# Kernel optimization log

Measured on AMD Instinct MI355X. Metric: run time of the kernel, lower is better.

## Reference

```python
import jax, jax.numpy as jnp
import numpy as np

SQRT_D = 16.0   # sqrt(d), d=256
BETA2 = 18.0    # beta^2 / 2, beta=6
EPS_BN = 1e-5


def _bn1d(x, g, b):
    # eval-mode BatchNorm1d with freshly-initialized running stats (mean=0, var=1)
    scale = g / jnp.sqrt(1.0 + EPS_BN)
    if x.ndim == 3:  # [B, C, N]
        return x * scale[:, None] + b[:, None]
    return x * scale + b  # [B, C]


def _crelu(z):
    return jax.nn.relu(z.real) + 1j * jax.nn.relu(z.imag)


def _sa_layer(x, qk_w, v_w, v_b, t_w, t_b, g, b):
    # x: [B, C, N]; q and k share weights (q_conv.weight = k_conv.weight)
    xq = jnp.einsum('oc,bcn->bno', qk_w, x)            # [B, N, C/4]
    xk = jnp.einsum('oc,bcn->bon', qk_w, x)            # [B, C/4, N]
    xv = jnp.einsum('oc,bcn->bon', v_w, x) + v_b[:, None]
    energy = jnp.einsum('bno,bom->bnm', xq, xk)        # [B, N, N]
    att = jax.nn.softmax(energy, axis=-1)
    att = att / (1e-9 + att.sum(axis=1, keepdims=True))  # sum-normalized over dim=1
    xr = jnp.einsum('bcn,bnm->bcm', xv, att)           # [B, C, N]
    xr = jax.nn.relu(_bn1d(jnp.einsum('oc,bcn->bon', t_w, x - xr) + t_b[:, None], g, b))
    return x + xr


def _forward(x, A, P, cl1_wr, cl1_wi, cl1_br, cl1_bi, cl2_wr, cl2_wi, cl2_br, cl2_bi,
             pt_conv1_w, pt_conv2_w, pt_bn1_g, pt_bn1_b, pt_bn2_g, pt_bn2_b,
             sa_qk_w, sa_v_w, sa_v_b, sa_t_w, sa_t_b, sa_bn_g, sa_bn_b,
             fuse_w, fuse_bn_g, fuse_bn_b, lin1_w, bn6_g, bn6_b,
             lin2_w, lin2_b, bn7_g, bn7_b, lin3_w, lin3_b):
    pts = jnp.transpose(x, (0, 2, 1))                  # [B, N, 3]
    # ---- VecKM: pairwise Gaussian kernel times complex random features ----
    sq = jnp.sum(pts * pts, axis=-1)                   # [B, N]
    D2 = sq[:, :, None] + sq[:, None, :] - 2.0 * jnp.einsum('bnc,bmc->bnm', pts, pts)
    J = jnp.exp(-BETA2 * D2).astype(jnp.complex64)     # [B, N, N]
    eA = jnp.exp(1j * (pts @ A))                       # [B, N, d] complex64
    G = (J @ eA) / eA
    G = G / jnp.linalg.norm(G, axis=-1, keepdims=True) * SQRT_D
    G = G + jnp.exp(1j * (pts @ P))                    # positional encoding
    # ---- ComplexLinear -> ComplexReLU -> ComplexLinear ----
    W1 = (cl1_wr + 1j * cl1_wi).astype(jnp.complex64)
    G = _crelu(G @ W1.T + (cl1_br + 1j * cl1_bi))
    W2 = (cl2_wr + 1j * cl2_wi).astype(jnp.complex64)
    G = G @ W2.T + (cl2_br + 1j * cl2_bi)
    Gr = G.real ** 2 + G.imag ** 2                     # [B, N, 256]
    Gc = jnp.transpose(Gr, (0, 2, 1))                  # [B, 256, N]
    # ---- Point_Transformer_Last ----
    h = jax.nn.relu(_bn1d(jnp.einsum('oc,bcn->bon', pt_conv1_w, Gc), pt_bn1_g, pt_bn1_b))
    h = jax.nn.relu(_bn1d(jnp.einsum('oc,bcn->bon', pt_conv2_w, h), pt_bn2_g, pt_bn2_b))
    feats = []
    for i in range(4):
        h = _sa_layer(h, sa_qk_w[i], sa_v_w[i], sa_v_b[i], sa_t_w[i], sa_t_b[i],
                      sa_bn_g[i], sa_bn_b[i])
        feats.append(h)
    h = jnp.concatenate(feats + [Gc], axis=1)          # [B, 1280, N]
    h = jax.nn.leaky_relu(_bn1d(jnp.einsum('oc,bcn->bon', fuse_w, h), fuse_bn_g, fuse_bn_b), 0.2)
    h = jnp.max(h, axis=-1)                            # adaptive_max_pool1d -> [B, 1024]
    h = jax.nn.leaky_relu(_bn1d(h @ lin1_w.T, bn6_g, bn6_b), 0.2)
    h = jax.nn.leaky_relu(_bn1d(h @ lin2_w.T + lin2_b, bn7_g, bn7_b), 0.2)
    return h @ lin3_w.T + lin3_b                       # [B, 40]


def setup_inputs() -> dict:
    key = jax.random.key(0)
    ks = iter(jax.random.split(key, 64))
    B, N, d = 16, 1024, 256
    r = lambda shape, s=0.05: jax.random.normal(next(ks), shape, dtype=jnp.float32) * s
    inp = {
        'x': jax.random.normal(next(ks), (B, 3, N), dtype=jnp.float32),
        'A': jax.random.normal(next(ks), (3, d), dtype=jnp.float32) * 30.0,
        'P': jax.random.normal(next(ks), (3, d), dtype=jnp.float32),
        'cl1_wr': r((d, d)), 'cl1_wi': r((d, d)), 'cl1_br': r((d,)), 'cl1_bi': r((d,)),
        'cl2_wr': r((d, d)), 'cl2_wi': r((d, d)), 'cl2_br': r((d,)), 'cl2_bi': r((d,)),
        'pt_conv1_w': r((256, 256)), 'pt_conv2_w': r((256, 256)),
        'pt_bn1_g': jnp.ones(256), 'pt_bn1_b': jnp.zeros(256),
        'pt_bn2_g': jnp.ones(256), 'pt_bn2_b': jnp.zeros(256),
        'sa_qk_w': r((4, 64, 256)), 'sa_v_w': r((4, 256, 256)), 'sa_v_b': r((4, 256)),
        'sa_t_w': r((4, 256, 256)), 'sa_t_b': r((4, 256)),
        'sa_bn_g': jnp.ones((4, 256)), 'sa_bn_b': jnp.zeros((4, 256)),
        'fuse_w': r((1024, 1280)), 'fuse_bn_g': jnp.ones(1024), 'fuse_bn_b': jnp.zeros(1024),
        'lin1_w': r((512, 1024)), 'bn6_g': jnp.ones(512), 'bn6_b': jnp.zeros(512),
        'lin2_w': r((256, 512)), 'lin2_b': r((256,)),
        'bn7_g': jnp.ones(256), 'bn7_b': jnp.zeros(256),
        'lin3_w': r((40, 256)), 'lin3_b': r((40,)),
    }
    return inp


def reference(x, A, P, cl1_wr, cl1_wi, cl1_br, cl1_bi, cl2_wr, cl2_wi, cl2_br, cl2_bi,
              pt_conv1_w, pt_conv2_w, pt_bn1_g, pt_bn1_b, pt_bn2_g, pt_bn2_b,
              sa_qk_w, sa_v_w, sa_v_b, sa_t_w, sa_t_b, sa_bn_g, sa_bn_b,
              fuse_w, fuse_bn_g, fuse_bn_b, lin1_w, bn6_g, bn6_b,
              lin2_w, lin2_b, bn7_g, bn7_b, lin3_w, lin3_b):
    return _forward(x, A, P, cl1_wr, cl1_wi, cl1_br, cl1_bi, cl2_wr, cl2_wi, cl2_br, cl2_bi,
                    pt_conv1_w, pt_conv2_w, pt_bn1_g, pt_bn1_b, pt_bn2_g, pt_bn2_b,
                    sa_qk_w, sa_v_w, sa_v_b, sa_t_w, sa_t_b, sa_bn_g, sa_bn_b,
                    fuse_w, fuse_bn_g, fuse_bn_b, lin1_w, bn6_g, bn6_b,
                    lin2_w, lin2_b, bn7_g, bn7_b, lin3_w, lin3_b)
```

## Files before the change

kernel.cpp:

```cpp
#include <hip/hip_runtime.h>
#include <math.h>

#define BB 16
#define NN 1024
#define DD 256

typedef unsigned short u16;
typedef unsigned int uint32;
typedef __attribute__((ext_vector_type(8))) short s8v;
typedef __attribute__((ext_vector_type(4))) float f4v;

__device__ __forceinline__ u16 f2b(float f) {
  uint32 u = __float_as_uint(f);
  return (u16)((u + 0x7fffu + ((u >> 16) & 1u)) >> 16);
}
__device__ __forceinline__ float b2f(u16 u) {
  return __uint_as_float(((uint32)u) << 16);
}

__device__ __forceinline__ float waveRedSum(float v) {
  #pragma unroll
  for (int o = 32; o; o >>= 1) v += __shfl_xor(v, o, 64);
  return v;
}
__device__ __forceinline__ float waveRedMax(float v) {
  #pragma unroll
  for (int o = 32; o; o >>= 1) v = fmaxf(v, __shfl_xor(v, o, 64));
  return v;
}

__global__ void k_pts(const float* __restrict__ x, float* __restrict__ pts) {
  int i = blockIdx.x * 256 + threadIdx.x;
  if (i >= BB * NN) return;
  int b = i >> 10, n = i & 1023;
  const float* xb = x + (size_t)b * 3 * NN;
  pts[i * 3 + 0] = xb[n];
  pts[i * 3 + 1] = xb[NN + n];
  pts[i * 3 + 2] = xb[2 * NN + n];
}

__global__ void k_phase(const float* __restrict__ pts, const float* __restrict__ A,
                        float2* __restrict__ eA) {
  int i = blockIdx.x * 256 + threadIdx.x;
  int d = i & 255; int bn = i >> 8;
  float p0 = pts[bn * 3], p1 = pts[bn * 3 + 1], p2 = pts[bn * 3 + 2];
  float ta = p0 * A[d] + p1 * A[256 + d] + p2 * A[512 + d];
  float s, c;
  sincosf(ta, &s, &c); eA[i] = make_float2(c, s);
}

__global__ void k_eat(const float2* __restrict__ eA, u16* __restrict__ eAT) {
  int bid = blockIdx.x;
  int dt = bid & 7, nt = (bid >> 3) & 15, b = bid >> 7;
  int d0 = dt * 32, n0 = nt * 64;
  __shared__ u16 cosT[32][72], sinT[32][72];
  int t = threadIdx.x;
  {
    int n = t >> 2, dg = (t & 3) * 8;
    const float2* p = eA + ((size_t)(b * 1024 + n0 + n)) * 256 + d0 + dg;
    #pragma unroll
    for (int j = 0; j < 8; j++) {
      float2 v = p[j];
      cosT[dg + j][n] = f2b(v.x);
      sinT[dg + j][n] = f2b(v.y);
    }
  }
  __syncthreads();
  {
    int rr = t >> 2, ng = (t & 3) * 16;
    int d = rr >> 1, cmp = rr & 1;
    const u16* src = (cmp ? &sinT[d][ng] : &cosT[d][ng]);
    uint4 v0 = *(const uint4*)src;
    uint4 v1 = *(const uint4*)(src + 8);
    u16* dst = eAT + ((size_t)(b * 512 + 2 * d0 + rr)) * 1024 + n0 + ng;
    *(uint4*)dst = v0;
    *(uint4*)(dst + 8) = v1;
  }
}

__global__ void k_jbuild(const float* __restrict__ pts, u16* __restrict__ J) {
  int bid = blockIdx.x;
  int b = bid >> 10, n = bid & 1023;
  int t = threadIdx.x;
  const float* pb = pts + (size_t)b * 3072;
  float pnx = pb[n * 3], pny = pb[n * 3 + 1], pnz = pb[n * 3 + 2];
  int m = t * 4;
  const float* pm = pb + (size_t)m * 3;
  float4 a = *(const float4*)pm;
  float4 bq = *(const float4*)(pm + 4);
  float4 c = *(const float4*)(pm + 8);
  float dx, dy, dz, d2;
  dx = a.x - pnx;  dy = a.y - pny;  dz = a.z - pnz;  d2 = dx*dx + dy*dy + dz*dz;
  float j0 = __expf(-18.0f * d2);
  dx = a.w - pnx;  dy = bq.x - pny; dz = bq.y - pnz; d2 = dx*dx + dy*dy + dz*dz;
  float j1 = __expf(-18.0f * d2);
  dx = bq.z - pnx; dy = bq.w - pny; dz = c.x - pnz;  d2 = dx*dx + dy*dy + dz*dz;
  float j2 = __expf(-18.0f * d2);
  dx = c.y - pnx;  dy = c.z - pny;  dz = c.w - pnz;  d2 = dx*dx + dy*dy + dz*dz;
  float j3 = __expf(-18.0f * d2);
  uint32 lo = (uint32)f2b(j0) | ((uint32)f2b(j1) << 16);
  uint32 hi = (uint32)f2b(j2) | ((uint32)f2b(j3) << 16);
  *(uint2*)(J + (size_t)bid * 1024 + m) = make_uint2(lo, hi);
}

__global__ void k_norm(const float2* __restrict__ M, const float2* __restrict__ eA,
                       const float* __restrict__ pts, const float* __restrict__ P,
                       u16* __restrict__ Gb) {
  int bn = blockIdx.x; int c = threadIdx.x;
  size_t idx = (size_t)bn * DD + c;
  float2 m = M[idx], e = eA[idx];
  float gr = m.x * e.x + m.y * e.y;
  float gi = m.y * e.x - m.x * e.y;
  float s = gr * gr + gi * gi;
  s = waveRedSum(s);
  __shared__ float red[4];
  if ((c & 63) == 0) red[c >> 6] = s;
  __syncthreads();
  float tot = red[0] + red[1] + red[2] + red[3];
  float scale = 16.0f / sqrtf(tot);
  float p0 = pts[bn * 3], p1 = pts[bn * 3 + 1], p2 = pts[bn * 3 + 2];
  float tp = p0 * P[c] + p1 * P[256 + c] + p2 * P[512 + c];
  float sp, cp; sincosf(tp, &sp, &cp);
  uint32 pk = (uint32)f2b(gr * scale + cp) | ((uint32)f2b(gi * scale + sp) << 16);
  *(uint32*)(Gb + idx * 2) = pk;
}

__global__ void k_cast(const float* __restrict__ s, u16* __restrict__ d, int n) {
  int i = blockIdx.x * 256 + threadIdx.x;
  if (i < n) d[i] = f2b(s[i]);
}
__global__ void k_wprep(const float* __restrict__ wr, const float* __restrict__ wi,
                        u16* __restrict__ dst) {
  int i = blockIdx.x * 256 + threadIdx.x;
  int op = i >> 9, c2 = i & 511, c = c2 >> 1, pl = c2 & 1;
  float v;
  if (op < 256) v = pl ? -wi[op * 256 + c] : wr[op * 256 + c];
  else          v = pl ?  wr[(op - 256) * 256 + c] : wi[(op - 256) * 256 + c];
  dst[i] = f2b(v);
}
__global__ void k_cbias(const float* __restrict__ br, const float* __restrict__ bi,
                        float* __restrict__ cb) {
  int t = threadIdx.x;
  cb[t] = (t < 256) ? br[t] : bi[t - 256];
}

__global__ void k_g2(const u16* __restrict__ G2b, u16* __restrict__ bigT) {
  int i = blockIdx.x * 256 + threadIdx.x;
  int row = i >> 8, c = i & 255;
  float re = b2f(G2b[(size_t)row * 512 + 2 * c]);
  float im = b2f(G2b[(size_t)row * 512 + 2 * c + 1]);
  bigT[(size_t)row * 1280 + 1024 + c] = f2b(re * re + im * im);
}

template<int BM>
__launch_bounds__(256)
__global__ void k_mm(const u16* __restrict__ Ab, long a_bs, int lda,
                     const u16* __restrict__ Btb, long b_bs, int ldb,
                     int K, int tiles_m, int tiles_n,
                     const float* __restrict__ bias,
                     const float* __restrict__ bng, const float* __restrict__ bnb,
                     const float* __restrict__ cbias,
                     int act,
                     const float* __restrict__ res, long res_bs, int res_sub,
                     float* __restrict__ outF, long outF_bs, int ldF,
                     u16* __restrict__ outB, long outB_bs, int ldBo, int ileave,
                     u16* __restrict__ outT, long outT_bs, int ldT) {
  constexpr int BN = 128;
  constexpr int WM = (BM == 128) ? 64 : 32;
  constexpr int MI = WM / 16;
  __shared__ u16 smem[BN * BM];
  u16* As = smem;
  u16* Bs = smem + BM * 32;
  int t = threadIdx.x;
  int l = t & 63, w = t >> 6;
  int p = l & 15, q = l >> 4;
  int bid = blockIdx.x;
  int tn = bid % tiles_n;
  int tm = (bid / tiles_n) % tiles_m;
  int b  = bid / (tiles_n * tiles_m);
  int m0 = tm * BM, n0 = tn * BN;
  int wm = w >> 1, wn = w & 1;
  const u16* Ap = Ab + (size_t)b * a_bs;
  const u16* Bp = Btb + (size_t)b * b_bs;

  f4v acc[MI][4];
  #pragma unroll
  for (int i = 0; i < MI; i++)
    #pragma unroll
    for (int j = 0; j < 4; j++) acc[i][j] = (f4v){0.f, 0.f, 0.f, 0.f};

  int arow = t >> 2, kg = (t & 3) * 8;
  for (int k0 = 0; k0 < K; k0 += 32) {
    __syncthreads();
    #pragma unroll
    for (int it = 0; it < BM / 64; it++) {
      int r = it * 64 + arow;
      float4 v = *(const float4*)(Ap + (size_t)(m0 + r) * lda + k0 + kg);
      *(float4*)&As[r * 32 + kg] = v;
    }
    #pragma unroll
    for (int it = 0; it < 2; it++) {
      int r = it * 64 + arow;
      float4 v = *(const float4*)(Bp + (size_t)(n0 + r) * ldb + k0 + kg);
      *(float4*)&Bs[r * 32 + kg] = v;
    }
    __syncthreads();
    s8v af[MI], bf[4];
    #pragma unroll
    for (int i = 0; i < MI; i++)
      af[i] = *(const s8v*)&As[(wm * WM + i * 16 + p) * 32 + q * 8];
    #pragma unroll
    for (int j = 0; j < 4; j++)
      bf[j] = *(const s8v*)&Bs[(wn * 64 + j * 16 + p) * 32 + q * 8];
    #pragma unroll
    for (int i = 0; i < MI; i++)
      #pragma unroll
      for (int j = 0; j < 4; j++)
        acc[i][j] = __builtin_amdgcn_mfma_f32_16x16x32_bf16(af[i], bf[j], acc[i][j], 0, 0, 0);
  }

  __syncthreads();

  float cbv[4];
  #pragma unroll
  for (int j = 0; j < 4; j++) {
    int no = n0 + wn * 64 + j * 16 + p;
    cbv[j] = cbias ? cbias[no] : 0.0f;
  }
  const float BNS = 0.99999500003749966f;
  #pragma unroll
  for (int i = 0; i < MI; i++) {
    #pragma unroll
    for (int r = 0; r < 4; r++) {
      int mo = m0 + wm * WM + i * 16 + q * 4 + r;
      float mult = 1.f, add = 0.f;
      if (bias) add = bias[mo];
      if (bng) { float s = bng[mo] * BNS; add = add * s + bnb[mo]; mult = s; }
      #pragma unroll
      for (int j = 0; j < 4; j++) {
        int no = n0 + wn * 64 + j * 16 + p;
        float v = acc[i][j][r];
        v = v * mult + add;
        if (cbias) v += cbv[j];
        if (act == 1) v = fmaxf(v, 0.f);
        else if (act == 2) v = v > 0.f ? v : 0.2f * v;
        if (res) {
          float rv = res[(size_t)b * res_bs + (size_t)mo * NN + no];
          v = res_sub ? rv - v : rv + v;
        }
        if (outF) outF[(size_t)b * outF_bs + (size_t)mo * ldF + no] = v;
        if (outB) {
          int noo = ileave ? (((no & 255) << 1) | (no >> 8)) : no;
          outB[(size_t)b * outB_bs + (size_t)mo * ldBo + noo] = f2b(v);
        }
        if (outT) smem[(wn * 64 + j * 16 + p) * BM + (mo - m0)] = f2b(v);
      }
    }
  }
  if (outT) {
    __syncthreads();
    constexpr int CPR = BM / 8;
    constexpr int RPP = 256 / CPR;
    int row0 = t / CPR, cg = (t % CPR) * 8;
    for (int rr = row0; rr < BN; rr += RPP) {
      float4 v = *(const float4*)&smem[rr * BM + cg];
      *(float4*)(outT + (size_t)b * outT_bs + (size_t)(n0 + rr) * ldT + m0 + cg) = v;
    }
  }
}

__global__ void k_rowstats(const float* __restrict__ E, float* __restrict__ rmax_,
                           float* __restrict__ rinv_) {
  int row = blockIdx.x;
  const float* pp = E + (size_t)row * NN;
  int t = threadIdx.x;
  float4 v = *(const float4*)(pp + t * 4);
  float mx = fmaxf(fmaxf(v.x, v.y), fmaxf(v.z, v.w));
  mx = waveRedMax(mx);
  __shared__ float redm[4];
  __shared__ float reds[4];
  if ((t & 63) == 0) redm[t >> 6] = mx;
  __syncthreads();
  mx = fmaxf(fmaxf(redm[0], redm[1]), fmaxf(redm[2], redm[3]));
  float s = __expf(v.x - mx) + __expf(v.y - mx) + __expf(v.z - mx) + __expf(v.w - mx);
  s = waveRedSum(s);
  if ((t & 63) == 0) reds[t >> 6] = s;
  __syncthreads();
  if (t == 0) {
    float tot = reds[0] + reds[1] + reds[2] + reds[3];
    rmax_[row] = mx;
    rinv_[row] = 1.0f / tot;
  }
}

__launch_bounds__(256)
__global__ void k_xratt(const u16* __restrict__ xv_, const float* __restrict__ E,
                        const float* __restrict__ rmax_, const float* __restrict__ rinv_,
                        const float* __restrict__ XinF, long xinF_bs,
                        u16* __restrict__ diffT) {
  __shared__ u16 smem[16384];
  __shared__ float colred[128][4];
  u16* As = smem;
  u16* Bs = smem + 4096;
  int t = threadIdx.x;
  int l = t & 63, w = t >> 6;
  int p = l & 15, q = l >> 4;
  int bid = blockIdx.x;
  int mt = bid & 7, ct = (bid >> 3) & 1, b = bid >> 4;
  int c0 = ct * 128, m0 = mt * 128;
  int wm = w >> 1, wn = w & 1;
  const u16* Ap = xv_ + (size_t)b * 262144;
  const float* Ep = E + ((size_t)b << 20);
  const float* rmx = rmax_ + (b << 10);
  const float* riv = rinv_ + (b << 10);
  f4v acc[4][4];
  #pragma unroll
  for (int i = 0; i < 4; i++)
    #pragma unroll
    for (int j = 0; j < 4; j++) acc[i][j] = (f4v){0.f, 0.f, 0.f, 0.f};
  float colpart0 = 0.f, colpart1 = 0.f;
  int arow = t >> 2, kg = (t & 3) * 8;
  for (int k0 = 0; k0 < 1024; k0 += 32) {
    __syncthreads();
    #pragma unroll
    for (int it = 0; it < 2; it++) {
      int r = it * 64 + arow;
      *(float4*)&As[r * 32 + kg] = *(const float4*)(Ap + (size_t)(c0 + r) * 1024 + k0 + kg);
    }
    float4 ma0 = *(const float4*)(rmx + k0 + kg);
    float4 ma1 = *(const float4*)(rmx + k0 + kg + 4);
    float4 ia0 = *(const float4*)(riv + k0 + kg);
    float4 ia1 = *(const float4*)(riv + k0 + kg + 4);
    #pragma unroll
    for (int it = 0; it < 2; it++) {
      int r = it * 64 + arow;
      const float* ep = Ep + (size_t)(m0 + r) * 1024 + k0 + kg;
      float4 e0 = *(const float4*)ep;
      float4 e1 = *(const float4*)(ep + 4);
      float p0 = __expf(e0.x - ma0.x) * ia0.x;
      float p1 = __expf(e0.y - ma0.y) * ia0.y;
      float p2 = __expf(e0.z - ma0.z) * ia0.z;
      float p3 = __expf(e0.w - ma0.w) * ia0.w;
      float p4 = __expf(e1.x - ma1.x) * ia1.x;
      float p5 = __expf(e1.y - ma1.y) * ia1.y;
      float p6 = __expf(e1.z - ma1.z) * ia1.z;
      float p7 = __expf(e1.w - ma1.w) * ia1.w;
      float s8 = ((p0 + p1) + (p2 + p3)) + ((p4 + p5) + (p6 + p7));
      if (it == 0) colpart0 += s8; else colpart1 += s8;
      uint32 w0 = (uint32)f2b(p0) | ((uint32)f2b(p1) << 16);
      uint32 w1 = (uint32)f2b(p2) | ((uint32)f2b(p3) << 16);
      uint32 w2 = (uint32)f2b(p4) | ((uint32)f2b(p5) << 16);
      uint32 w3 = (uint32)f2b(p6) | ((uint32)f2b(p7) << 16);
      *(uint4*)&Bs[r * 32 + kg] = make_uint4(w0, w1, w2, w3);
    }
    __syncthreads();
    s8v af[4], bf[4];
    #pragma unroll
    for (int i = 0; i < 4; i++)
      af[i] = *(const s8v*)&As[(wm * 64 + i * 16 + p) * 32 + q * 8];
    #pragma unroll
    for (int j = 0; j < 4; j++)
      bf[j] = *(const s8v*)&Bs[(wn * 64 + j * 16 + p) * 32 + q * 8];
    #pragma unroll
    for (int i = 0; i < 4; i++)
      #pragma unroll
      for (int j = 0; j < 4; j++)
        acc[i][j] = __builtin_amdgcn_mfma_f32_16x16x32_bf16(af[i], bf[j], acc[i][j], 0, 0, 0);
  }
  colred[arow][t & 3] = colpart0;
  colred[64 + arow][t & 3] = colpart1;
  __syncthreads();
  float csv[4];
  #pragma unroll
  for (int j = 0; j < 4; j++) {
    int ml = wn * 64 + j * 16 + p;
    csv[j] = 1.0f / (1e-9f + colred[ml][0] + colred[ml][1] + colred[ml][2] + colred[ml][3]);
  }
  #pragma unroll
  for (int i = 0; i < 4; i++) {
    #pragma unroll
    for (int r = 0; r < 4; r++) {
      int cl = wm * 64 + i * 16 + q * 4 + r;
      int c = c0 + cl;
      #pragma unroll
      for (int j = 0; j < 4; j++) {
        int ml = wn * 64 + j * 16 + p;
        float v = acc[i][j][r] * csv[j];
        float rv = XinF[(size_t)b * xinF_bs + (size_t)c * 1024 + m0 + ml];
        smem[ml * 128 + cl] = f2b(rv - v);
      }
    }
  }
  __syncthreads();
  int rr0 = t >> 4, cg = (t & 15) * 8;
  #pragma unroll
  for (int k = 0; k < 8; k++) {
    int rr = rr0 + k * 16;
    *(float4*)(diffT + (size_t)b * 262144 + (size_t)(m0 + rr) * 256 + c0 + cg) =
        *(const float4*)&smem[rr * 128 + cg];
  }
}

__global__ void k_maxpool(const float* __restrict__ fin, float* __restrict__ pool) {
  int bo = blockIdx.x;
  const float* pp = fin + (size_t)bo * NN;
  int t = threadIdx.x;
  float m = fmaxf(fmaxf(pp[t], pp[t + 256]), fmaxf(pp[t + 512], pp[t + 768]));
  m = waveRedMax(m);
  __shared__ float red[4];
  if ((t & 63) == 0) red[t >> 6] = m;
  __syncthreads();
  if (t == 0) pool[bo] = fmaxf(fmaxf(red[0], red[1]), fmaxf(red[2], red[3]));
}

__global__ void k_fc(const float* __restrict__ in, int Cc,
                     const float* __restrict__ W,
                     const float* __restrict__ bias,
                     const float* __restrict__ bng, const float* __restrict__ bnb,
                     int act, float* __restrict__ out, int O) {
  int i = blockIdx.x * 256 + threadIdx.x;
  if (i >= BB * O) return;
  int b = i / O, o = i % O;
  const float* xp = in + (size_t)b * Cc;
  const float* wp = W + (size_t)o * Cc;
  float s = 0.f;
  for (int c = 0; c < Cc; c += 4) {
    float4 xv = *(const float4*)(xp + c);
    float4 wv = *(const float4*)(wp + c);
    s += xv.x * wv.x + xv.y * wv.y + xv.z * wv.z + xv.w * wv.w;
  }
  if (bias) s += bias[o];
  const float BNS = 0.99999500003749966f;
  if (bng) s = s * (bng[o] * BNS) + bnb[o];
  if (act == 2) s = s > 0.f ? s : 0.2f * s;
  else if (act == 1) s = fmaxf(s, 0.f);
  out[i] = s;
}

extern "C" void kernel_launch(void* const* d_in, const int* in_sizes, int n_in,
                              void* d_out, int out_size, void* d_ws, size_t ws_size,
                              hipStream_t stream) {
  const float* x        = (const float*)d_in[0];
  const float* A        = (const float*)d_in[1];
  const float* P        = (const float*)d_in[2];
  const float* cl1_wr   = (const float*)d_in[3];
  const float* cl1_wi   = (const float*)d_in[4];
  const float* cl1_br   = (const float*)d_in[5];
  const float* cl1_bi   = (const float*)d_in[6];
  const float* cl2_wr   = (const float*)d_in[7];
  const float* cl2_wi   = (const float*)d_in[8];
  const float* cl2_br   = (const float*)d_in[9];
  const float* cl2_bi   = (const float*)d_in[10];
  const float* pt_c1_w  = (const float*)d_in[11];
  const float* pt_c2_w  = (const float*)d_in[12];
  const float* pt_bn1_g = (const float*)d_in[13];
  const float* pt_bn1_b = (const float*)d_in[14];
  const float* pt_bn2_g = (const float*)d_in[15];
  const float* pt_bn2_b = (const float*)d_in[16];
  const float* sa_qk_w  = (const float*)d_in[17];
  const float* sa_v_w   = (const float*)d_in[18];
  const float* sa_v_b   = (const float*)d_in[19];
  const float* sa_t_w   = (const float*)d_in[20];
  const float* sa_t_b   = (const float*)d_in[21];
  const float* sa_bn_g  = (const float*)d_in[22];
  const float* sa_bn_b  = (const float*)d_in[23];
  const float* fuse_w   = (const float*)d_in[24];
  const float* fuse_g   = (const float*)d_in[25];
  const float* fuse_b   = (const float*)d_in[26];
  const float* lin1_w   = (const float*)d_in[27];
  const float* bn6_g    = (const float*)d_in[28];
  const float* bn6_b    = (const float*)d_in[29];
  const float* lin2_w   = (const float*)d_in[30];
  const float* lin2_b   = (const float*)d_in[31];
  const float* bn7_g    = (const float*)d_in[32];
  const float* bn7_b    = (const float*)d_in[33];
  const float* lin3_w   = (const float*)d_in[34];
  const float* lin3_b   = (const float*)d_in[35];

  float* ws = (float*)d_ws;
  const size_t oPts  = 0;
  const size_t oS    = 65536;
  const size_t oBigT = oS + 16777216;
  const size_t oXf0  = oBigT + 10485760;
  const size_t oXf1  = oXf0 + 4194304;
  const size_t oH1T  = oXf1 + 4194304;
  const size_t oH2T  = oH1T + 2097152;
  const size_t oXkT  = oH2T + 2097152;
  const size_t oXv   = oXkT + 524288;
  const size_t oAux  = oXv + 2097152;
  const size_t oGb   = oAux + 8388608;
  const size_t oW1c  = oGb + 4194304;
  const size_t oW2c  = oW1c + 131072;
  const size_t oCb1  = oW2c + 131072;
  const size_t oCb2  = oCb1 + 512;
  const size_t oPool = oCb2 + 512;
  const size_t oFc1  = oPool + 16384;
  const size_t oFc2  = oFc1 + 8192;
  const size_t oWp   = oFc2 + 4096;

  float*  pts  = ws + oPts;
  float2* eA   = (float2*)(ws + oS);
  float2* Mj   = (float2*)(ws + oS + 8388608);
  u16*    G1b  = (u16*)(ws + oS);
  u16*    G2b  = (u16*)(ws + oS + 8388608);
  float*  Ebuf = ws + oS;
  float*  fuseO= ws + oS;
  u16*    bigT = (u16*)(ws + oBigT);
  float*  Xf0  = ws + oXf0;
  float*  Xf1  = ws + oXf1;
  u16*    h1T  = (u16*)(ws + oH1T);
  u16*    diffT= (u16*)(ws + oH1T);
  u16*    h2T  = (u16*)(ws + oH2T);
  u16*    xkT  = (u16*)(ws + oXkT);
  u16*    xv   = (u16*)(ws + oXv);
  u16*    eAT  = (u16*)(ws + oAux);
  u16*    Jb   = (u16*)(ws + oAux + 4194304);
  float*  rmax = ws + oAux;
  float*  rinv = ws + oAux + 16384;
  u16*    Gb   = (u16*)(ws + oGb);
  u16*    W1c  = (u16*)(ws + oW1c);
  u16*    W2c  = (u16*)(ws + oW2c);
  float*  cb1  = ws + oCb1;
  float*  cb2  = ws + oCb2;
  float*  pool = ws + oPool;
  float*  fc1  = ws + oFc1;
  float*  fc2  = ws + oFc2;
  u16*    wp   = (u16*)(ws + oWp);
  u16* wp_pt1  = wp;
  u16* wp_pt2  = wp + 65536;
  u16* wp_qk   = wp + 131072;
  u16* wp_v    = wp + 196608;
  u16* wp_t    = wp + 458752;
  u16* wp_fuse = wp + 720896;

  k_cast<<<256, 256, 0, stream>>>(pt_c1_w, wp_pt1, 65536);
  k_cast<<<256, 256, 0, stream>>>(pt_c2_w, wp_pt2, 65536);
  k_cast<<<256, 256, 0, stream>>>(sa_qk_w, wp_qk, 65536);
  k_cast<<<1024, 256, 0, stream>>>(sa_v_w, wp_v, 262144);
  k_cast<<<1024, 256, 0, stream>>>(sa_t_w, wp_t, 262144);
  k_cast<<<5120, 256, 0, stream>>>(fuse_w, wp_fuse, 1310720);
  k_wprep<<<1024, 256, 0, stream>>>(cl1_wr, cl1_wi, W1c);
  k_wprep<<<1024, 256, 0, stream>>>(cl2_wr, cl2_wi, W2c);
  k_cbias<<<1, 512, 0, stream>>>(cl1_br, cl1_bi, cb1);
  k_cbias<<<1, 512, 0, stream>>>(cl2_br, cl2_bi, cb2);

  k_pts<<<64, 256, 0, stream>>>(x, pts);
  k_phase<<<16384, 256, 0, stream>>>(pts, A, eA);
  k_eat<<<2048, 256, 0, stream>>>(eA, eAT);
  k_jbuild<<<16384, 256, 0, stream>>>(pts, Jb);
  k_mm<128><<<512, 256, 0, stream>>>(Jb, 1048576, 1024, eAT, 524288, 1024, 1024, 8, 4,
      nullptr, nullptr, nullptr, nullptr, 0, nullptr, 0, 0,
      (float*)Mj, 524288, 512, nullptr, 0, 0, 0, nullptr, 0, 0);
  k_norm<<<BB * NN, 256, 0, stream>>>(Mj, eA, pts, P, Gb);

  k_mm<128><<<512, 256, 0, stream>>>(Gb, 0, 512, W1c, 0, 512, 512, 128, 4,
      nullptr, nullptr, nullptr, cb1, 1, nullptr, 0, 0,
      nullptr, 0, 0, G1b, 0, 512, 1, nullptr, 0, 0);
  k_mm<128><<<512, 256, 0, stream>>>(G1b, 0, 512, W2c, 0, 512, 512, 128, 4,
      nullptr, nullptr, nullptr, cb2, 0, nullptr, 0, 0,
      nullptr, 0, 0, G2b, 0, 512, 1, nullptr, 0, 0);
  k_g2<<<16384, 256, 0, stream>>>(G2b, bigT);

  const long bsBigT = 1310720;
  const long bsH256 = 262144;
  const long bsXkT  = 65536;
  const long bsXvU  = 262144;
  const long bsF    = 262144;
  const long bsE    = 1048576;

  k_mm<128><<<256, 256, 0, stream>>>(wp_pt1, 0, 256, bigT + 1024, bsBigT, 1280, 256, 2, 8,
      nullptr, pt_bn1_g, pt_bn1_b, nullptr, 1, nullptr, 0, 0,
      nullptr, 0, 0, nullptr, 0, 0, 0, h1T, bsH256, 256);
  k_mm<128><<<256, 256, 0, stream>>>(wp_pt2, 0, 256, h1T, bsH256, 256, 256, 2, 8,
      nullptr, pt_bn2_g, pt_bn2_b, nullptr, 1, nullptr, 0, 0,
      Xf0, bsF, 1024, nullptr, 0, 0, 0, h2T, bsH256, 256);

  for (int i = 0; i < 4; i++) {
    const u16* XinT   = (i == 0) ? h2T : (bigT + (i - 1) * 256);
    long       xinT_bs= (i == 0) ? bsH256 : bsBigT;
    int        xinT_ld= (i == 0) ? 256 : 1280;
    float*     XinF   = (i & 1) ? Xf1 : Xf0;
    float*     XoutF  = (i & 1) ? Xf0 : Xf1;
    const u16* qkw = wp_qk + (size_t)i * 16384;
    const u16* vw  = wp_v + (size_t)i * 65536;
    const u16* tw  = wp_t + (size_t)i * 65536;

    k_mm<64><<<128, 256, 0, stream>>>(qkw, 0, 256, XinT, xinT_bs, xinT_ld, 256, 1, 8,
        nullptr, nullptr, nullptr, nullptr, 0, nullptr, 0, 0,
        nullptr, 0, 0, nullptr, 0, 0, 0, xkT, bsXkT, 64);
    k_mm<128><<<256, 256, 0, stream>>>(vw, 0, 256, XinT, xinT_bs, xinT_ld, 256, 2, 8,
        sa_v_b + i * 256, nullptr, nullptr, nullptr, 0, nullptr, 0, 0,
        nullptr, 0, 0, xv, bsXvU, 1024, 0, nullptr, 0, 0);
    k_mm<128><<<1024, 256, 0, stream>>>(xkT, bsXkT, 64, xkT, bsXkT, 64, 64, 8, 8,
        nullptr, nullptr, nullptr, nullptr, 0, nullptr, 0, 0,
        Ebuf, bsE, 1024, nullptr, 0, 0, 0, nullptr, 0, 0);
    k_rowstats<<<BB * NN, 256, 0, stream>>>(Ebuf, rmax, rinv);
    k_xratt<<<256, 256, 0, stream>>>(xv, Ebuf, rmax, rinv, XinF, bsF, diffT);
    k_mm<128><<<256, 256, 0, stream>>>(tw, 0, 256, diffT, bsH256, 256, 256, 2, 8,
        sa_t_b + i * 256, sa_bn_g + i * 256, sa_bn_b + i * 256, nullptr, 1,
        XinF, bsF, 0,
        XoutF, bsF, 1024, nullptr, 0, 0, 0, bigT + i * 256, bsBigT, 1280);
  }

  k_mm<128><<<1024, 256, 0, stream>>>(wp_fuse, 0, 1280, bigT, bsBigT, 1280, 1280, 8, 8,
      nullptr, fuse_g, fuse_b, nullptr, 2, nullptr, 0, 0,
      fuseO, 1048576, 1024, nullptr, 0, 0, 0, nullptr, 0, 0);
  k_maxpool<<<BB * 1024, 256, 0, stream>>>(fuseO, pool);

  k_fc<<<32, 256, 0, stream>>>(pool, 1024, lin1_w, nullptr, bn6_g, bn6_b, 2, fc1, 512);
  k_fc<<<16, 256, 0, stream>>>(fc1, 512, lin2_w, lin2_b, bn7_g, bn7_b, 2, fc2, 256);
  k_fc<<<3, 256, 0, stream>>>(fc2, 256, lin3_w, lin3_b, nullptr, nullptr, 0, (float*)d_out, 40);
}
```

Measured before the change: 1.096 ms.

## Recompute attention energy on the fly and fuse max-pool into fuse GEMM

The full N×N energy matrix is no longer written to memory. Row softmax statistics now come from a tiled MFMA kernel that emits per-tile partial max/sum, followed by a small combine kernel. The attention-times-value kernel recomputes energy tiles from xkT with MFMA instead of reading the stored fp32 energy. The fuse GEMM reduces its output tile to per-row maxima, so the 1024-wide fuse output is never stored, and a tiny kernel finishes the pool. LDS rows in the GEMM are padded to reduce bank conflicts. The cost is redundant energy MFMA work and more kernel complexity.

After: 1.535 ms. 1.4x slower.

```diff
diff --git a/kernel.cpp b/kernel.cpp
--- a/kernel.cpp
+++ b/kernel.cpp
@@ -164,13 +164,15 @@
                      const float* __restrict__ res, long res_bs, int res_sub,
                      float* __restrict__ outF, long outF_bs, int ldF,
                      u16* __restrict__ outB, long outB_bs, int ldBo, int ileave,
-                     u16* __restrict__ outT, long outT_bs, int ldT) {
+                     u16* __restrict__ outT, long outT_bs, int ldT,
+                     float* __restrict__ outPool) {
   constexpr int BN = 128;
   constexpr int WM = (BM == 128) ? 64 : 32;
   constexpr int MI = WM / 16;
-  __shared__ u16 smem[BN * BM];
+  constexpr int TLD = BM + 8;
+  __shared__ u16 smem[BN * TLD];
   u16* As = smem;
-  u16* Bs = smem + BM * 32;
+  u16* Bs = smem + BM * 36;
   int t = threadIdx.x;
   int l = t & 63, w = t >> 6;
   int p = l & 15, q = l >> 4;
@@ -196,22 +198,22 @@
     for (int it = 0; it < BM / 64; it++) {
       int r = it * 64 + arow;
       float4 v = *(const float4*)(Ap + (size_t)(m0 + r) * lda + k0 + kg);
-      *(float4*)&As[r * 32 + kg] = v;
+      *(float4*)&As[r * 36 + kg] = v;
     }
     #pragma unroll
     for (int it = 0; it < 2; it++) {
       int r = it * 64 + arow;
       float4 v = *(const float4*)(Bp + (size_t)(n0 + r) * ldb + k0 + kg);
-      *(float4*)&Bs[r * 32 + kg] = v;
+      *(float4*)&Bs[r * 36 + kg] = v;
     }
     __syncthreads();
     s8v af[MI], bf[4];
     #pragma unroll
     for (int i = 0; i < MI; i++)
-      af[i] = *(const s8v*)&As[(wm * WM + i * 16 + p) * 32 + q * 8];
+      af[i] = *(const s8v*)&As[(wm * WM + i * 16 + p) * 36 + q * 8];
     #pragma unroll
     for (int j = 0; j < 4; j++)
-      bf[j] = *(const s8v*)&Bs[(wn * 64 + j * 16 + p) * 32 + q * 8];
+      bf[j] = *(const s8v*)&Bs[(wn * 64 + j * 16 + p) * 36 + q * 8];
     #pragma unroll
     for (int i = 0; i < MI; i++)
       #pragma unroll
@@ -227,6 +229,11 @@
     int no = n0 + wn * 64 + j * 16 + p;
     cbv[j] = cbias ? cbias[no] : 0.0f;
   }
+  float pmax[MI][4];
+  #pragma unroll
+  for (int i = 0; i < MI; i++)
+    #pragma unroll
+    for (int r = 0; r < 4; r++) pmax[i][r] = -3.0e38f;
   const float BNS = 0.99999500003749966f;
   #pragma unroll
   for (int i = 0; i < MI; i++) {
@@ -248,12 +255,13 @@
           float rv = res[(size_t)b * res_bs + (size_t)mo * NN + no];
           v = res_sub ? rv - v : rv + v;
         }
+        if (outPool) pmax[i][r] = fmaxf(pmax[i][r], v);
         if (outF) outF[(size_t)b * outF_bs + (size_t)mo * ldF + no] = v;
         if (outB) {
           int noo = ileave ? (((no & 255) << 1) | (no >> 8)) : no;
           outB[(size_t)b * outB_bs + (size_t)mo * ldBo + noo] = f2b(v);
         }
-        if (outT) smem[(wn * 64 + j * 16 + p) * BM + (mo - m0)] = f2b(v);
+        if (outT) smem[(wn * 64 + j * 16 + p) * TLD + (mo - m0)] = f2b(v);
       }
     }
   }
@@ -263,121 +271,228 @@
     constexpr int RPP = 256 / CPR;
     int row0 = t / CPR, cg = (t % CPR) * 8;
     for (int rr = row0; rr < BN; rr += RPP) {
-      float4 v = *(const float4*)&smem[rr * BM + cg];
+      float4 v = *(const float4*)&smem[rr * TLD + cg];
       *(float4*)(outT + (size_t)b * outT_bs + (size_t)(n0 + rr) * ldT + m0 + cg) = v;
     }
   }
-}
-
-__global__ void k_rowstats(const float* __restrict__ E, float* __restrict__ rmax_,
-                           float* __restrict__ rinv_) {
-  int row = blockIdx.x;
-  const float* pp = E + (size_t)row * NN;
-  int t = threadIdx.x;
-  float4 v = *(const float4*)(pp + t * 4);
-  float mx = fmaxf(fmaxf(v.x, v.y), fmaxf(v.z, v.w));
-  mx = waveRedMax(mx);
-  __shared__ float redm[4];
-  __shared__ float reds[4];
-  if ((t & 63) == 0) redm[t >> 6] = mx;
-  __syncthreads();
-  mx = fmaxf(fmaxf(redm[0], redm[1]), fmaxf(redm[2], redm[3]));
-  float s = __expf(v.x - mx) + __expf(v.y - mx) + __expf(v.z - mx) + __expf(v.w - mx);
-  s = waveRedSum(s);
-  if ((t & 63) == 0) reds[t >> 6] = s;
-  __syncthreads();
-  if (t == 0) {
-    float tot = reds[0] + reds[1] + reds[2] + reds[3];
-    rmax_[row] = mx;
-    rinv_[row] = 1.0f / tot;
+  if (outPool) {
+    float* pf = (float*)smem;
+    #pragma unroll
+    for (int i = 0; i < MI; i++)
+      #pragma unroll
+      for (int r = 0; r < 4; r++) {
+        float m = pmax[i][r];
+        #pragma unroll
+        for (int o = 1; o < 16; o <<= 1) m = fmaxf(m, __shfl_xor(m, o, 64));
+        if (p == 0) pf[(wm * WM + i * 16 + q * 4 + r) * 2 + wn] = m;
+      }
+    __syncthreads();
+    if (t < BM) {
+      float mv = fmaxf(pf[t * 2], pf[t * 2 + 1]);
+      outPool[((size_t)b * (tiles_m * BM) + m0 + t) * tiles_n + tn] = mv;
+    }
   }
 }
 
 __launch_bounds__(256)
-__global__ void k_xratt(const u16* __restrict__ xv_, const float* __restrict__ E,
-                        const float* __restrict__ rmax_, const float* __restrict__ rinv_,
-                        const float* __restrict__ XinF, long xinF_bs,
-                        u16* __restrict__ diffT) {
-  __shared__ u16 smem[16384];
-  __shared__ float colred[128][4];
-  u16* As = smem;
-  u16* Bs = smem + 4096;
+__global__ void k_estats(const u16* __restrict__ xkT_, float* __restrict__ part) {
+  __shared__ u16 As[128 * 72];
+  __shared__ u16 Bs[128 * 72];
+  __shared__ float lred[128][2];
+  __shared__ float gm[128];
+  __shared__ float lsum[128][2];
   int t = threadIdx.x;
   int l = t & 63, w = t >> 6;
   int p = l & 15, q = l >> 4;
+  int wm = w >> 1, wn = w & 1;
+  int bid = blockIdx.x;
+  int ct = bid & 7, rt = (bid >> 3) & 7, b = bid >> 6;
+  const u16* xkp = xkT_ + (size_t)b * 65536;
+  {
+    int kg = (t & 7) * 8;
+    int r0 = t >> 3;
+    #pragma unroll
+    for (int it = 0; it < 4; it++) {
+      int r = it * 32 + r0;
+      *(float4*)&As[r * 72 + kg] = *(const float4*)(xkp + (size_t)(rt * 128 + r) * 64 + kg);
+      *(float4*)&Bs[r * 72 + kg] = *(const float4*)(xkp + (size_t)(ct * 128 + r) * 64 + kg);
+    }
+  }
+  __syncthreads();
+  f4v acc[4][4];
+  #pragma unroll
+  for (int i = 0; i < 4; i++)
+    #pragma unroll
+    for (int j = 0; j < 4; j++) acc[i][j] = (f4v){0.f, 0.f, 0.f, 0.f};
+  #pragma unroll
+  for (int ks = 0; ks < 2; ks++) {
+    int ko = ks * 32 + q * 8;
+    s8v af[4], bf[4];
+    #pragma unroll
+    for (int i = 0; i < 4; i++)
+      af[i] = *(const s8v*)&As[(wm * 64 + i * 16 + p) * 72 + ko];
+    #pragma unroll
+    for (int j = 0; j < 4; j++)
+      bf[j] = *(const s8v*)&Bs[(wn * 64 + j * 16 + p) * 72 + ko];
+    #pragma unroll
+    for (int i = 0; i < 4; i++)
+      #pragma unroll
+      for (int j = 0; j < 4; j++)
+        acc[i][j] = __builtin_amdgcn_mfma_f32_16x16x32_bf16(af[i], bf[j], acc[i][j], 0, 0, 0);
+  }
+  #pragma unroll
+  for (int i = 0; i < 4; i++)
+    #pragma unroll
+    for (int r = 0; r < 4; r++) {
+      float m = fmaxf(fmaxf(acc[i][0][r], acc[i][1][r]), fmaxf(acc[i][2][r], acc[i][3][r]));
+      #pragma unroll
+      for (int o = 1; o < 16; o <<= 1) m = fmaxf(m, __shfl_xor(m, o, 64));
+      if (p == 0) lred[wm * 64 + i * 16 + q * 4 + r][wn] = m;
+    }
+  __syncthreads();
+  if (t < 128) gm[t] = fmaxf(lred[t][0], lred[t][1]);
+  __syncthreads();
+  #pragma unroll
+  for (int i = 0; i < 4; i++)
+    #pragma unroll
+    for (int r = 0; r < 4; r++) {
+      int row = wm * 64 + i * 16 + q * 4 + r;
+      float g = gm[row];
+      float s = __expf(acc[i][0][r] - g) + __expf(acc[i][1][r] - g) +
+                __expf(acc[i][2][r] - g) + __expf(acc[i][3][r] - g);
+      #pragma unroll
+      for (int o = 1; o < 16; o <<= 1) s += __shfl_xor(s, o, 64);
+      if (p == 0) lsum[row][wn] = s;
+    }
+  __syncthreads();
+  if (t < 128) {
+    float2 v = make_float2(gm[t], lsum[t][0] + lsum[t][1]);
+    *(float2*)(part + (((size_t)b * 1024 + rt * 128 + t) * 8 + ct) * 2) = v;
+  }
+}
+
+__global__ void k_scomb(const float* __restrict__ part, float* __restrict__ rmax_,
+                        float* __restrict__ rinv_) {
+  int i = blockIdx.x * 256 + threadIdx.x;
+  const float2* pp = (const float2*)(part + (size_t)i * 16);
+  float2 v[8];
+  #pragma unroll
+  for (int k = 0; k < 8; k++) v[k] = pp[k];
+  float g = v[0].x;
+  #pragma unroll
+  for (int k = 1; k < 8; k++) g = fmaxf(g, v[k].x);
+  float s = 0.f;
+  #pragma unroll
+  for (int k = 0; k < 8; k++) s += v[k].y * __expf(v[k].x - g);
+  rmax_[i] = g;
+  rinv_[i] = 1.0f / s;
+}
+
+__launch_bounds__(256)
+__global__ void k_xratt2(const u16* __restrict__ xv_, const u16* __restrict__ xkT_,
+                         const float* __restrict__ rmax_, const float* __restrict__ rinv_,
+                         const float* __restrict__ XinF, long xinF_bs,
+                         u16* __restrict__ diffT) {
+  __shared__ u16 pool[20736];
+  __shared__ float colred[128][2];
+  u16* Km = pool;
+  u16* Kn = pool + 9216;
+  u16* As = pool + 11520;
+  u16* Bs = pool + 16128;
+  int t = threadIdx.x;
+  int l = t & 63, w = t >> 6;
+  int p = l & 15, q = l >> 4;
+  int wm = w >> 1, wn = w & 1;
   int bid = blockIdx.x;
   int mt = bid & 7, ct = (bid >> 3) & 1, b = bid >> 4;
   int c0 = ct * 128, m0 = mt * 128;
-  int wm = w >> 1, wn = w & 1;
-  const u16* Ap = xv_ + (size_t)b * 262144;
-  const float* Ep = E + ((size_t)b << 20);
+  const u16* xvp = xv_ + (size_t)b * 262144;
+  const u16* xkp = xkT_ + (size_t)b * 65536;
   const float* rmx = rmax_ + (b << 10);
   const float* riv = rinv_ + (b << 10);
+  {
+    int kg = (t & 7) * 8;
+    int r0 = t >> 3;
+    #pragma unroll
+    for (int it = 0; it < 4; it++) {
+      int r = it * 32 + r0;
+      *(float4*)&Km[r * 72 + kg] = *(const float4*)(xkp + (size_t)(m0 + r) * 64 + kg);
+    }
+  }
   f4v acc[4][4];
+  float colp[4][4];
   #pragma unroll
   for (int i = 0; i < 4; i++)
     #pragma unroll
-    for (int j = 0; j < 4; j++) acc[i][j] = (f4v){0.f, 0.f, 0.f, 0.f};
-  float colpart0 = 0.f, colpart1 = 0.f;
-  int arow = t >> 2, kg = (t & 3) * 8;
+    for (int j = 0; j < 4; j++) { acc[i][j] = (f4v){0.f, 0.f, 0.f, 0.f}; colp[i][j] = 0.f; }
   for (int k0 = 0; k0 < 1024; k0 += 32) {
     __syncthreads();
-    #pragma unroll
-    for (int it = 0; it < 2; it++) {
-      int r = it * 64 + arow;
-      *(float4*)&As[r * 32 + kg] = *(const float4*)(Ap + (size_t)(c0 + r) * 1024 + k0 + kg);
-    }
-    float4 ma0 = *(const float4*)(rmx + k0 + kg);
-    float4 ma1 = *(const float4*)(rmx + k0 + kg + 4);
-    float4 ia0 = *(const float4*)(riv + k0 + kg);
-    float4 ia1 = *(const float4*)(riv + k0 + kg + 4);
-    #pragma unroll
-    for (int it = 0; it < 2; it++) {
-      int r = it * 64 + arow;
-      const float* ep = Ep + (size_t)(m0 + r) * 1024 + k0 + kg;
-      float4 e0 = *(const float4*)ep;
-      float4 e1 = *(const float4*)(ep + 4);
-      float p0 = __expf(e0.x - ma0.x) * ia0.x;
-      float p1 = __expf(e0.y - ma0.y) * ia0.y;
-      float p2 = __expf(e0.z - ma0.z) * ia0.z;
-      float p3 = __expf(e0.w - ma0.w) * ia0.w;
-      float p4 = __expf(e1.x - ma1.x) * ia1.x;
-      float p5 = __expf(e1.y - ma1.y) * ia1.y;
-      float p6 = __expf(e1.z - ma1.z) * ia1.z;
-      float p7 = __expf(e1.w - ma1.w) * ia1.w;
-      float s8 = ((p0 + p1) + (p2 + p3)) + ((p4 + p5) + (p6 + p7));
-      if (it == 0) colpart0 += s8; else colpart1 += s8;
-      uint32 w0 = (uint32)f2b(p0) | ((uint32)f2b(p1) << 16);
-      uint32 w1 = (uint32)f2b(p2) | ((uint32)f2b(p3) << 16);
-      uint32 w2 = (uint32)f2b(p4) | ((uint32)f2b(p5) << 16);
-      uint32 w3 = (uint32)f2b(p6) | ((uint32)f2b(p7) << 16);
-      *(uint4*)&Bs[r * 32 + kg] = make_uint4(w0, w1, w2, w3);
-    }
+    {
+      int r0 = t >> 2, kg = (t & 3) * 8;
+      #pragma unroll
+      for (int it = 0; it < 2; it++) {
+        int r = it * 64 + r0;
+        *(float4*)&As[r * 36 + kg] = *(const float4*)(xvp + (size_t)(c0 + r) * 1024 + k0 + kg);
+      }
+    }
+    {
+      int row = t >> 3, kg = (t & 7) * 8;
+      *(float4*)&Kn[row * 72 + kg] = *(const float4*)(xkp + (size_t)(k0 + row) * 64 + kg);
+    }
+    __syncthreads();
+    f4v Ef[4];
+    s8v be0 = *(const s8v*)&Kn[(wn * 16 + p) * 72 + q * 8];
+    s8v be1 = *(const s8v*)&Kn[(wn * 16 + p) * 72 + 32 + q * 8];
+    #pragma unroll
+    for (int i = 0; i < 4; i++) {
+      s8v a0 = *(const s8v*)&Km[(wm * 64 + i * 16 + p) * 72 + q * 8];
+      s8v a1 = *(const s8v*)&Km[(wm * 64 + i * 16 + p) * 72 + 32 + q * 8];
+      Ef[i] = __builtin_amdgcn_mfma_f32_16x16x32_bf16(a0, be0, (f4v){0.f, 0.f, 0.f, 0.f}, 0, 0, 0);
+      Ef[i] = __builtin_amdgcn_mfma_f32_16x16x32_bf16(a1, be1, Ef[i], 0, 0, 0);
+    }
+    int n = k0 + wn * 16 + p;
+    float rm = rmx[n], ri = riv[n];
+    #pragma unroll
+    for (int i = 0; i < 4; i++)
+      #pragma unroll
+      for (int r = 0; r < 4; r++) {
+        float pv = __expf(Ef[i][r] - rm) * ri;
+        colp[i][r] += pv;
+        Bs[(wm * 64 + i * 16 + q * 4 + r) * 36 + wn * 16 + p] = f2b(pv);
+      }
     __syncthreads();
     s8v af[4], bf[4];
     #pragma unroll
     for (int i = 0; i < 4; i++)
-      af[i] = *(const s8v*)&As[(wm * 64 + i * 16 + p) * 32 + q * 8];
+      af[i] = *(const s8v*)&As[(wm * 64 + i * 16 + p) * 36 + q * 8];
     #pragma unroll
     for (int j = 0; j < 4; j++)
-      bf[j] = *(const s8v*)&Bs[(wn * 64 + j * 16 + p) * 32 + q * 8];
+      bf[j] = *(const s8v*)&Bs[(wn * 64 + j * 16 + p) * 36 + q * 8];
     #pragma unroll
     for (int i = 0; i < 4; i++)
       #pragma unroll
       for (int j = 0; j < 4; j++)
         acc[i][j] = __builtin_amdgcn_mfma_f32_16x16x32_bf16(af[i], bf[j], acc[i][j], 0, 0, 0);
   }
-  colred[arow][t & 3] = colpart0;
-  colred[64 + arow][t & 3] = colpart1;
+  #pragma unroll
+  for (int i = 0; i < 4; i++)
+    #pragma unroll
+    for (int r = 0; r < 4; r++) {
+      float s = colp[i][r];
+      #pragma unroll
+      for (int o = 1; o < 16; o <<= 1) s += __shfl_xor(s, o, 64);
+      if (p == 0) colred[wm * 64 + i * 16 + q * 4 + r][wn] = s;
+    }
   __syncthreads();
   float csv[4];
   #pragma unroll
   for (int j = 0; j < 4; j++) {
-    int ml = wn * 64 + j * 16 + p;
-    csv[j] = 1.0f / (1e-9f + colred[ml][0] + colred[ml][1] + colred[ml][2] + colred[ml][3]);
-  }
-  #pragma unroll
-  for (int i = 0; i < 4; i++) {
+    int no = wn * 64 + j * 16 + p;
+    csv[j] = 1.0f / (1e-9f + colred[no][0] + colred[no][1]);
+  }
+  u16* T = pool;
+  #pragma unroll
+  for (int i = 0; i < 4; i++)
     #pragma unroll
     for (int r = 0; r < 4; r++) {
       int cl = wm * 64 + i * 16 + q * 4 + r;
@@ -387,30 +502,25 @@
         int ml = wn * 64 + j * 16 + p;
         float v = acc[i][j][r] * csv[j];
         float rv = XinF[(size_t)b * xinF_bs + (size_t)c * 1024 + m0 + ml];
-        smem[ml * 128 + cl] = f2b(rv - v);
+        T[ml * 136 + cl] = f2b(rv - v);
       }
     }
-  }
   __syncthreads();
   int rr0 = t >> 4, cg = (t & 15) * 8;
   #pragma unroll
   for (int k = 0; k < 8; k++) {
     int rr = rr0 + k * 16;
     *(float4*)(diffT + (size_t)b * 262144 + (size_t)(m0 + rr) * 256 + c0 + cg) =
-        *(const float4*)&smem[rr * 128 + cg];
-  }
-}
-
-__global__ void k_maxpool(const float* __restrict__ fin, float* __restrict__ pool) {
-  int bo = blockIdx.x;
-  const float* pp = fin + (size_t)bo * NN;
-  int t = threadIdx.x;
-  float m = fmaxf(fmaxf(pp[t], pp[t + 256]), fmaxf(pp[t + 512], pp[t + 768]));
-  m = waveRedMax(m);
-  __shared__ float red[4];
-  if ((t & 63) == 0) red[t >> 6] = m;
-  __syncthreads();
-  if (t == 0) pool[bo] = fmaxf(fmaxf(red[0], red[1]), fmaxf(red[2], red[3]));
+        *(const float4*)&T[rr * 136 + cg];
+  }
+}
+
+__global__ void k_pool8(const float* __restrict__ pp, float* __restrict__ pool) {
+  int i = blockIdx.x * 256 + threadIdx.x;
+  const float4* p4 = (const float4*)(pp + (size_t)i * 8);
+  float4 a = p4[0], b = p4[1];
+  pool[i] = fmaxf(fmaxf(fmaxf(a.x, a.y), fmaxf(a.z, a.w)),
+                  fmaxf(fmaxf(b.x, b.y), fmaxf(b.z, b.w)));
 }
 
 __global__ void k_fc(const float* __restrict__ in, int Cc,
@@ -503,8 +613,8 @@
   float2* Mj   = (float2*)(ws + oS + 8388608);
   u16*    G1b  = (u16*)(ws + oS);
   u16*    G2b  = (u16*)(ws + oS + 8388608);
-  float*  Ebuf = ws + oS;
-  float*  fuseO= ws + oS;
+  float*  partP= ws + oS;
+  float*  poolP= ws + oS + 262144;
   u16*    bigT = (u16*)(ws + oBigT);
   float*  Xf0  = ws + oXf0;
   float*  Xf1  = ws + oXf1;
@@ -550,15 +660,15 @@
   k_jbuild<<<16384, 256, 0, stream>>>(pts, Jb);
   k_mm<128><<<512, 256, 0, stream>>>(Jb, 1048576, 1024, eAT, 524288, 1024, 1024, 8, 4,
       nullptr, nullptr, nullptr, nullptr, 0, nullptr, 0, 0,
-      (float*)Mj, 524288, 512, nullptr, 0, 0, 0, nullptr, 0, 0);
+      (float*)Mj, 524288, 512, nullptr, 0, 0, 0, nullptr, 0, 0, nullptr);
   k_norm<<<BB * NN, 256, 0, stream>>>(Mj, eA, pts, P, Gb);
 
   k_mm<128><<<512, 256, 0, stream>>>(Gb, 0, 512, W1c, 0, 512, 512, 128, 4,
       nullptr, nullptr, nullptr, cb1, 1, nullptr, 0, 0,
-      nullptr, 0, 0, G1b, 0, 512, 1, nullptr, 0, 0);
+      nullptr, 0, 0, G1b, 0, 512, 1, nullptr, 0, 0, nullptr);
   k_mm<128><<<512, 256, 0, stream>>>(G1b, 0, 512, W2c, 0, 512, 512, 128, 4,
       nullptr, nullptr, nullptr, cb2, 0, nullptr, 0, 0,
-      nullptr, 0, 0, G2b, 0, 512, 1, nullptr, 0, 0);
+      nullptr, 0, 0, G2b, 0, 512, 1, nullptr, 0, 0, nullptr);
   k_g2<<<16384, 256, 0, stream>>>(G2b, bigT);
 
   const long bsBigT = 1310720;
@@ -566,14 +676,13 @@
   const long bsXkT  = 65536;
   const long bsXvU  = 262144;
   const long bsF    = 262144;
-  const long bsE    = 1048576;
 
   k_mm<128><<<256, 256, 0, stream>>>(wp_pt1, 0, 256, bigT + 1024, bsBigT, 1280, 256, 2, 8,
       nullptr, pt_bn1_g, pt_bn1_b, nullptr, 1, nullptr, 0, 0,
-      nullptr, 0, 0, nullptr, 0, 0, 0, h1T, bsH256, 256);
+      nullptr, 0, 0, nullptr, 0, 0, 0, h1T, bsH256, 256, nullptr);
   k_mm<128><<<256, 256, 0, stream>>>(wp_pt2, 0, 256, h1T, bsH256, 256, 256, 2, 8,
       nullptr, pt_bn2_g, pt_bn2_b, nullptr, 1, nullptr, 0, 0,
-      Xf0, bsF, 1024, nullptr, 0, 0, 0, h2T, bsH256, 256);
+      Xf0, bsF, 1024, nullptr, 0, 0, 0, h2T, bsH256, 256, nullptr);
 
   for (int i = 0; i < 4; i++) {
     const u16* XinT   = (i == 0) ? h2T : (bigT + (i - 1) * 256);
@@ -587,25 +696,23 @@
 
     k_mm<64><<<128, 256, 0, stream>>>(qkw, 0, 256, XinT, xinT_bs, xinT_ld, 256, 1, 8,
         nullptr, nullptr, nullptr, nullptr, 0, nullptr, 0, 0,
-        nullptr, 0, 0, nullptr, 0, 0, 0, xkT, bsXkT, 64);
+        nullptr, 0, 0, nullptr, 0, 0, 0, xkT, bsXkT, 64, nullptr);
+    k_estats<<<1024, 256, 0, stream>>>(xkT, partP);
+    k_scomb<<<64, 256, 0, stream>>>(partP, rmax, rinv);
     k_mm<128><<<256, 256, 0, stream>>>(vw, 0, 256, XinT, xinT_bs, xinT_ld, 256, 2, 8,
         sa_v_b + i * 256, nullptr, nullptr, nullptr, 0, nullptr, 0, 0,
-        nullptr, 0, 0, xv, bsXvU, 1024, 0, nullptr, 0, 0);
-    k_mm<128><<<1024, 256, 0, stream>>>(xkT, bsXkT, 64, xkT, bsXkT, 64, 64, 8, 8,
-        nullptr, nullptr, nullptr, nullptr, 0, nullptr, 0, 0,
-        Ebuf, bsE, 1024, nullptr, 0, 0, 0, nullptr, 0, 0);
-    k_rowstats<<<BB * NN, 256, 0, stream>>>(Ebuf, rmax, rinv);
-    k_xratt<<<256, 256, 0, stream>>>(xv, Ebuf, rmax, rinv, XinF, bsF, diffT);
+        nullptr, 0, 0, xv, bsXvU, 1024, 0, nullptr, 0, 0, nullptr);
+    k_xratt2<<<256, 256, 0, stream>>>(xv, xkT, rmax, rinv, XinF, bsF, diffT);
     k_mm<128><<<256, 256, 0, stream>>>(tw, 0, 256, diffT, bsH256, 256, 256, 2, 8,
         sa_t_b + i * 256, sa_bn_g + i * 256, sa_bn_b + i * 256, nullptr, 1,
         XinF, bsF, 0,
-        XoutF, bsF, 1024, nullptr, 0, 0, 0, bigT + i * 256, bsBigT, 1280);
+        XoutF, bsF, 1024, nullptr, 0, 0, 0, bigT + i * 256, bsBigT, 1280, nullptr);
   }
 
   k_mm<128><<<1024, 256, 0, stream>>>(wp_fuse, 0, 1280, bigT, bsBigT, 1280, 1280, 8, 8,
       nullptr, fuse_g, fuse_b, nullptr, 2, nullptr, 0, 0,
-      fuseO, 1048576, 1024, nullptr, 0, 0, 0, nullptr, 0, 0);
-  k_maxpool<<<BB * 1024, 256, 0, stream>>>(fuseO, pool);
+      nullptr, 0, 0, nullptr, 0, 0, 0, nullptr, 0, 0, poolP);
+  k_pool8<<<64, 256, 0, stream>>>(poolP, pool);
 
   k_fc<<<32, 256, 0, stream>>>(pool, 1024, lin1_w, nullptr, bn6_g, bn6_b, 2, fc1, 512);
   k_fc<<<16, 256, 0, stream>>>(fc1, 512, lin2_w, lin2_b, bn7_g, bn7_b, 2, fc2, 256);
```
